# Kernel tuning notes

Hardware: AMD Instinct MI355X
Metric: run time of the kernel (lower is better)

## Reference

```python
import jax, jax.numpy as jnp
import numpy as np

NUM_HEADS = 8
CH_PER_HEAD = 40
NORM_GROUPS = 32
EPS = 1e-5


def setup_inputs() -> dict:
    key = jax.random.key(0)
    ks = jax.random.split(key, 8)
    B, C, H, W = 2, 320, 48, 48
    hid = NUM_HEADS * CH_PER_HEAD  # 320
    w_std = 0.02
    return {
        "x": jax.random.normal(ks[0], (B, C, H, W), dtype=jnp.float32),
        "gamma": jnp.ones((C,), dtype=jnp.float32),
        "beta": jnp.zeros((C,), dtype=jnp.float32),
        "Wq": jax.random.normal(ks[1], (hid, C), dtype=jnp.float32) * w_std,
        "bq": jax.random.normal(ks[2], (hid,), dtype=jnp.float32) * w_std,
        "Wk": jax.random.normal(ks[3], (hid, C), dtype=jnp.float32) * w_std,
        "bk": jax.random.normal(ks[4], (hid,), dtype=jnp.float32) * w_std,
        "Wv": jax.random.normal(ks[5], (hid, C), dtype=jnp.float32) * w_std,
        "bv": jax.random.normal(ks[6], (hid,), dtype=jnp.float32) * w_std,
        "Wo": jax.random.normal(ks[7], (C, hid), dtype=jnp.float32) * w_std,
        "bo": jnp.zeros((C,), dtype=jnp.float32),
    }


def _group_norm(x, gamma, beta):
    # x: [B, C, H, W]; GroupNorm over (C//G, H, W) per group, affine per-channel.
    B, C, H, W = x.shape
    xg = x.reshape(B, NORM_GROUPS, C // NORM_GROUPS, H, W)
    mean = xg.mean(axis=(2, 3, 4), keepdims=True)
    var = xg.var(axis=(2, 3, 4), keepdims=True)
    xn = ((xg - mean) * jax.lax.rsqrt(var + EPS)).reshape(B, C, H, W)
    return xn * gamma[None, :, None, None] + beta[None, :, None, None]


def reference(x, gamma, beta, Wq, bq, Wk, bk, Wv, bv, Wo, bo):
    B, C, H, W = x.shape
    N = H * W
    h, d = NUM_HEADS, CH_PER_HEAD
    scale = d ** (-0.25)  # applied to both q and k (net 1/sqrt(d))

    xn = _group_norm(x, gamma, beta).reshape(B, C, N)  # embedding = x_n (self-attn)

    # 1x1 Conv1d == matmul over channel dim
    q = jnp.einsum('oc,bcn->bon', Wq, xn) + bq[None, :, None]
    k = jnp.einsum('oc,bcn->bon', Wk, xn) + bk[None, :, None]
    v = jnp.einsum('oc,bcn->bon', Wv, xn) + bv[None, :, None]

    # b (h d) n -> b h d n
    q = q.reshape(B, h, d, N)
    k = k.reshape(B, h, d, N)
    v = v.reshape(B, h, d, N)

    attn = jax.nn.softmax(
        jnp.einsum('bhdi,bhdj->bhij', q * scale, k * scale), axis=-1
    )  # [B, h, N, N]
    out = jnp.einsum('bhij,bhdj->bhdi', attn, v).reshape(B, h * d, N)

    out = jnp.einsum('oc,bcn->bon', Wo, out) + bo[None, :, None]
    out = out.reshape(B, C, H, W)
    return x + out  # shapes match -> residual
```

## Files before the change

### kernel.cpp

```cpp
#include <hip/hip_runtime.h>
#include <hip/hip_bf16.h>

#define C_DIM   320
#define N_SP    2304
#define NHEADS  8
#define DHEAD   40
#define GROUPS  32
#define CPG     10
#define BATCH   2
#define DPAD    64
#define VPAD    48
#define W_ELEMS (C_DIM * C_DIM)
#define NSPLIT  3
#define TILES_PER_SPLIT 12
#define PSLOTS  41

typedef __bf16 bf16x8 __attribute__((ext_vector_type(8)));
typedef __bf16 bf16x4 __attribute__((ext_vector_type(4)));
typedef __bf16 bf16x2 __attribute__((ext_vector_type(2)));
typedef float  f32x4  __attribute__((ext_vector_type(4)));

typedef const __attribute__((address_space(1))) void* gas_ptr;
typedef __attribute__((address_space(3))) void* las_ptr;

#define MFMA16(a, b, c) __builtin_amdgcn_mfma_f32_16x16x32_bf16((a), (b), (c), 0, 0, 0)

#if __has_builtin(__builtin_amdgcn_exp2f)
#define EXP2(x) __builtin_amdgcn_exp2f(x)
#else
#define EXP2(x) __expf((x) * 0.6931471805599453f)
#endif

__device__ __forceinline__ void stage8(const char* gbase, char* lbase,
                                       int chunk, int lane)
{
    const int row = chunk * 8 + (lane >> 3);
    const int cs  = (lane & 7) * 16;
    __builtin_amdgcn_global_load_lds(
        (gas_ptr)(gbase + (size_t)row * (C_DIM * 2) + (cs ^ ((row & 7) << 4))),
        (las_ptr)(lbase + chunk * 1024 + lane * 16), 16, 0, 0);
}

__device__ __forceinline__ bf16x8 lds_frag(const char* lbase, int row, int cbyte)
{
    return *(const bf16x8*)(lbase + row * 128 + (cbyte ^ ((row & 7) << 4)));
}

__global__ __launch_bounds__(256) void prep_kernel(
    const float* __restrict__ x, float* __restrict__ partials,
    const float* __restrict__ Wq, const float* __restrict__ Wk,
    const float* __restrict__ Wv, const float* __restrict__ Wo,
    __bf16* __restrict__ Wqb, __bf16* __restrict__ Wkb,
    __bf16* __restrict__ Wvb, __bf16* __restrict__ Wob,
    __bf16* __restrict__ Qt, __bf16* __restrict__ Kt, __bf16* __restrict__ Vb)
{
    if (blockIdx.x < 512) {
        const int bid = blockIdx.x;
        const int bg = bid >> 3, p = bid & 7;
        const int b = bg >> 5, g = bg & 31;
        const float* xp = x + ((size_t)b * C_DIM + g * CPG) * N_SP + p * 288;
        const int tid = threadIdx.x;

        float sum = 0.f, sq = 0.f;
        #pragma unroll
        for (int c = 0; c < CPG; ++c) {
            for (int nl = tid; nl < 288; nl += 256) {
                const float v = xp[(size_t)c * N_SP + nl];
                sum += v; sq += v * v;
            }
        }
        #pragma unroll
        for (int off = 32; off; off >>= 1) {
            sum += __shfl_xor(sum, off);
            sq  += __shfl_xor(sq, off);
        }
        __shared__ float red[2][4];
        if ((tid & 63) == 0) { red[0][tid >> 6] = sum; red[1][tid >> 6] = sq; }
        __syncthreads();
        if (tid == 0) {
            partials[2 * bid]     = red[0][0] + red[0][1] + red[0][2] + red[0][3];
            partials[2 * bid + 1] = red[1][0] + red[1][1] + red[1][2] + red[1][3];
        }
    } else if (blockIdx.x < 612) {
        const int i = ((blockIdx.x - 512) * 256 + threadIdx.x) * 4;
        f32x4 a;
        bf16x4 o;
        a = *(const f32x4*)(Wq + i);
        #pragma unroll
        for (int e = 0; e < 4; ++e) o[e] = (__bf16)a[e];
        *(bf16x4*)(Wqb + i) = o;
        a = *(const f32x4*)(Wk + i);
        #pragma unroll
        for (int e = 0; e < 4; ++e) o[e] = (__bf16)a[e];
        *(bf16x4*)(Wkb + i) = o;
        a = *(const f32x4*)(Wv + i);
        #pragma unroll
        for (int e = 0; e < 4; ++e) o[e] = (__bf16)a[e];
        *(bf16x4*)(Wvb + i) = o;
        a = *(const f32x4*)(Wo + i);
        #pragma unroll
        for (int e = 0; e < 4; ++e) o[e] = (__bf16)a[e];
        *(bf16x4*)(Wob + i) = o;
    } else {
        const int t = (blockIdx.x - 612) * 256 + threadIdx.x;
        const bf16x8 z = {};
        __bf16* q = Qt + (size_t)t * DPAD + 40;
        __bf16* k = Kt + (size_t)t * DPAD + 40;
        *(bf16x8*)(q) = z; *(bf16x8*)(q + 8) = z; *(bf16x8*)(q + 16) = z;
        *(bf16x8*)(k) = z; *(bf16x8*)(k + 8) = z; *(bf16x8*)(k + 16) = z;
        const int bh = t / N_SP;
        const int rem = t - bh * N_SP;
        const int r = rem / 288, n8 = rem - r * 288;
        bf16x8 v = z;
        if (r == 0) {
            #pragma unroll
            for (int e = 0; e < 8; ++e) v[e] = (__bf16)1.0f;
        }
        *(bf16x8*)(Vb + ((size_t)bh * VPAD + 40 + r) * N_SP + n8 * 8) = v;
    }
}

__global__ __launch_bounds__(256) void gn_apply(
    const float* __restrict__ x,
    const float* __restrict__ gamma, const float* __restrict__ beta,
    const float* __restrict__ partials, __bf16* __restrict__ xn_t)
{
    const int bid = blockIdx.x;
    const int bg = bid >> 3, p = bid & 7;
    const int b = bg >> 5, g = bg & 31;
    const int c0 = g * CPG;

    float sum = 0.f, sq = 0.f;
    #pragma unroll
    for (int i = 0; i < 8; ++i) {
        sum += partials[(bg * 8 + i) * 2];
        sq  += partials[(bg * 8 + i) * 2 + 1];
    }
    const float inv_n = 1.0f / (float)(CPG * N_SP);
    const float mean = sum * inv_n;
    const float rstd = rsqrtf(sq * inv_n - mean * mean + 1e-5f);

    float ga[CPG], be[CPG];
    #pragma unroll
    for (int c = 0; c < CPG; ++c) {
        ga[c] = gamma[c0 + c] * rstd;
        be[c] = beta[c0 + c] - mean * ga[c];
    }

    const float* xp = x + ((size_t)b * C_DIM + c0) * N_SP + p * 288;
    for (int nl = threadIdx.x; nl < 288; nl += 256) {
        const int n = p * 288 + nl;
        __bf16* dst = xn_t + ((size_t)b * N_SP + n) * C_DIM + c0;
        #pragma unroll
        for (int j = 0; j < CPG / 2; ++j) {
            const float v0 = xp[(size_t)(2 * j) * N_SP + nl]     * ga[2 * j]     + be[2 * j];
            const float v1 = xp[(size_t)(2 * j + 1) * N_SP + nl] * ga[2 * j + 1] + be[2 * j + 1];
            bf16x2 t; t[0] = (__bf16)v0; t[1] = (__bf16)v1;
            *(bf16x2*)(dst + 2 * j) = t;
        }
    }
}

__global__ __launch_bounds__(256) void gemm_qkv(
    const __bf16* __restrict__ Wqb, const __bf16* __restrict__ Wkb, const __bf16* __restrict__ Wvb,
    const float* __restrict__ bq, const float* __restrict__ bk, const float* __restrict__ bv,
    const __bf16* __restrict__ Xt,
    __bf16* __restrict__ Qt, __bf16* __restrict__ Kt, __bf16* __restrict__ Vb)
{
    __shared__ __align__(16) char Ws[2][64 * 128];
    __shared__ __align__(16) char Xs[2][64 * 128];

    const int z = blockIdx.z;
    const int b = z / 3;
    const int which = z - 3 * b;
    const __bf16* W   = (which == 0) ? Wqb : (which == 1) ? Wkb : Wvb;
    const float* bias = (which == 0) ? bq : (which == 1) ? bk : bv;
    const float scale = (which == 0) ? 0.15811388300841897f
                      : (which == 1) ? 0.22811243f : 1.0f;

    const int n0 = blockIdx.x * 64, o0 = blockIdx.y * 64;
    const int tid = threadIdx.x, wave = tid >> 6, lane = tid & 63;
    const int lr = lane & 15, lk = lane >> 4;
    const int wm = wave >> 1, wn = wave & 1;

    const char* Wg = (const char*)(W + (size_t)o0 * C_DIM);
    const char* Xg = (const char*)(Xt + ((size_t)b * N_SP + n0) * C_DIM);

    auto stage = [&](int bufi, int s) {
        const int kb = s * 128;
        #pragma unroll
        for (int i = 0; i < 4; ++i) {
            const int c = wave * 4 + i;
            if (c < 8) stage8(Wg + kb, Ws[bufi], c, lane);
            else       stage8(Xg + kb, Xs[bufi], c - 8, lane);
        }
    };

    f32x4 acc[2][2] = {};

    stage(0, 0);
    __syncthreads();

    for (int s = 0; s < 5; ++s) {
        const int bufi = s & 1;
        if (s + 1 < 5) stage(bufi ^ 1, s + 1);

        const char* ws = Ws[bufi];
        const char* xs = Xs[bufi];
        __builtin_amdgcn_s_setprio(1);
        #pragma unroll
        for (int ksub = 0; ksub < 2; ++ksub) {
            const int cb = ksub * 64 + lk * 16;
            const bf16x8 a0 = lds_frag(ws, wm * 32 + lr,      cb);
            const bf16x8 a1 = lds_frag(ws, wm * 32 + 16 + lr, cb);
            const bf16x8 b0 = lds_frag(xs, wn * 32 + lr,      cb);
            const bf16x8 b1 = lds_frag(xs, wn * 32 + 16 + lr, cb);
            acc[0][0] = MFMA16(a0, b0, acc[0][0]);
            acc[0][1] = MFMA16(a0, b1, acc[0][1]);
            acc[1][0] = MFMA16(a1, b0, acc[1][0]);
            acc[1][1] = MFMA16(a1, b1, acc[1][1]);
        }
        __builtin_amdgcn_s_setprio(0);
        __syncthreads();
    }

    #pragma unroll
    for (int am = 0; am < 2; ++am) {
        #pragma unroll
        for (int rp = 0; rp < 2; ++rp) {
            const int o = o0 + wm * 32 + am * 16 + 4 * lk + 2 * rp;
            const int h = o / DHEAD, d = o - h * DHEAD;
            const int bh = b * NHEADS + h;
            const float b0_ = bias[o], b1_ = bias[o + 1];
            #pragma unroll
            for (int bn = 0; bn < 2; ++bn) {
                const int n = n0 + wn * 32 + bn * 16 + lr;
                const float v0 = (acc[am][bn][2 * rp]     + b0_) * scale;
                const float v1 = (acc[am][bn][2 * rp + 1] + b1_) * scale;
                if (which < 2) {
                    __bf16* dst = ((which == 0) ? Qt : Kt)
                                + ((size_t)bh * N_SP + n) * DPAD + d;
                    bf16x2 t; t[0] = (__bf16)v0; t[1] = (__bf16)v1;
                    *(bf16x2*)dst = t;
                } else {
                    Vb[((size_t)bh * VPAD + d)     * N_SP + n] = (__bf16)v0;
                    Vb[((size_t)bh * VPAD + d + 1) * N_SP + n] = (__bf16)v1;
                }
            }
        }
    }
}

__global__ __launch_bounds__(256) void gemm_out32(
    const __bf16* __restrict__ Wob, const float* __restrict__ bo,
    const __bf16* __restrict__ att_t,
    float* __restrict__ Y, const float* __restrict__ resid)
{
    __shared__ __align__(16) char Ws[2][32 * 128];
    __shared__ __align__(16) char Xs[2][64 * 128];

    const int b = blockIdx.z;
    const int n0 = blockIdx.x * 64, o0 = blockIdx.y * 32;
    const int tid = threadIdx.x, wave = tid >> 6, lane = tid & 63;
    const int lr = lane & 15, lk = lane >> 4;
    const int wn = wave;

    const char* Wg = (const char*)(Wob + (size_t)o0 * C_DIM);
    const char* Xg = (const char*)(att_t + ((size_t)b * N_SP + n0) * C_DIM);

    auto stage = [&](int bufi, int s) {
        const int kb = s * 128;
        #pragma unroll
        for (int i = 0; i < 3; ++i) {
            const int c = wave * 3 + i;
            if (c < 4) stage8(Wg + kb, Ws[bufi], c, lane);
            else       stage8(Xg + kb, Xs[bufi], c - 4, lane);
        }
    };

    f32x4 acc[2] = {};

    stage(0, 0);
    __syncthreads();

    for (int s = 0; s < 5; ++s) {
        const int bufi = s & 1;
        if (s + 1 < 5) stage(bufi ^ 1, s + 1);

        const char* ws = Ws[bufi];
        const char* xs = Xs[bufi];
        __builtin_amdgcn_s_setprio(1);
        #pragma unroll
        for (int ksub = 0; ksub < 2; ++ksub) {
            const int cb = ksub * 64 + lk * 16;
            const bf16x8 a0 = lds_frag(ws, lr,      cb);
            const bf16x8 a1 = lds_frag(ws, 16 + lr, cb);
            const bf16x8 b0 = lds_frag(xs, wn * 16 + lr, cb);
            acc[0] = MFMA16(a0, b0, acc[0]);
            acc[1] = MFMA16(a1, b0, acc[1]);
        }
        __builtin_amdgcn_s_setprio(0);
        __syncthreads();
    }

    const int n = n0 + wn * 16 + lr;
    #pragma unroll
    for (int am = 0; am < 2; ++am) {
        #pragma unroll
        for (int r = 0; r < 4; ++r) {
            const int o = o0 + am * 16 + 4 * lk + r;
            const size_t idx = ((size_t)b * C_DIM + o) * N_SP + n;
            Y[idx] = acc[am][r] + bo[o] + resid[idx];
        }
    }
}

__global__ __launch_bounds__(256, 4) void attn_mfma(
    const __bf16* __restrict__ Qt,
    const __bf16* __restrict__ Kt,
    const __bf16* __restrict__ Vb,
    __bf16* __restrict__ part)
{
    __shared__ __align__(16) __bf16 Ks[2][64 * DPAD];
    __shared__ __align__(16) __bf16 Vs[2][VPAD * 64];
    __shared__ __align__(16) __bf16 Ps[4][16 * 64];

    const int flat = blockIdx.x;
    const int bh = ((flat & 7) << 1) | ((flat >> 3) & 1);
    const int rest = flat >> 4;
    const int qx = rest / 3;
    const int s  = rest - 3 * qx;
    const int tid = threadIdx.x, wave = tid >> 6, lane = tid & 63;
    const int lr = lane & 15, lk = lane >> 4;
    const int swz = (lr & 7) << 4;
    const int i0 = (qx * 4 + wave) * 32;

    const char* Kg = (const char*)(Kt + (size_t)bh * N_SP * DPAD);
    const char* Vg = (const char*)(Vb + (size_t)bh * VPAD * N_SP);

    bf16x8 qb[2][2];
    #pragma unroll
    for (int qh = 0; qh < 2; ++qh) {
        const __bf16* Qp = Qt + ((size_t)bh * N_SP + i0 + qh * 16 + lr) * DPAD + lk * 8;
        qb[qh][0] = *(const bf16x8*)(Qp);
        qb[qh][1] = *(const bf16x8*)(Qp + 32);
    }

    f32x4 O[2][3] = {};

    auto stage = [&](char* kd, char* vd, int t) {
        const int j0 = t * 64;
        #pragma unroll
        for (int i2 = 0; i2 < 2; ++i2) {
            const int chunk = wave * 2 + i2;
            const int L = chunk * 1024 + lane * 16;
            const int src = L ^ (((L >> 7) & 7) << 4);
            __builtin_amdgcn_global_load_lds(
                (gas_ptr)(Kg + (size_t)j0 * 128 + src),
                (las_ptr)(kd + chunk * 1024), 16, 0, 0);
        }
        for (int i2 = wave; i2 < 6; i2 += 4) {
            const int row = i2 * 8 + (lane >> 3);
            const int csw = ((lane & 7) << 4) ^ ((row & 7) << 4);
            __builtin_amdgcn_global_load_lds(
                (gas_ptr)(Vg + ((size_t)row * N_SP + j0) * 2 + csw),
                (las_ptr)(vd + i2 * 1024), 16, 0, 0);
        }
    };

    auto compute = [&](const char* ks, const char* vs) {
        char* ps = (char*)Ps[wave];

        f32x4 S[2][4];
        __builtin_amdgcn_s_setprio(1);
        #pragma unroll
        for (int kt = 0; kt < 4; ++kt) {
            const int rowb = (kt * 16 + lr) * 128;
            const bf16x8 k0 = *(const bf16x8*)(ks + rowb + ((lk * 16) ^ swz));
            const bf16x8 k1 = *(const bf16x8*)(ks + rowb + ((64 + lk * 16) ^ swz));
            #pragma unroll
            for (int qh = 0; qh < 2; ++qh) {
                f32x4 zz = {};
                zz = MFMA16(k0, qb[qh][0], zz);
                S[qh][kt] = MFMA16(k1, qb[qh][1], zz);
            }
        }
        __builtin_amdgcn_s_setprio(0);

        bf16x8 va[2][3];
        #pragma unroll
        for (int hh = 0; hh < 2; ++hh)
            #pragma unroll
            for (int dt = 0; dt < 3; ++dt)
                va[hh][dt] = *(const bf16x8*)(vs + (dt * 16 + lr) * 128
                                              + ((hh * 64 + lk * 16) ^ swz));

        #pragma unroll
        for (int qh = 0; qh < 2; ++qh) {
            #pragma unroll
            for (int kt = 0; kt < 4; ++kt) {
                bf16x4 w;
                #pragma unroll
                for (int r = 0; r < 4; ++r)
                    w[r] = (__bf16)EXP2(S[qh][kt][r]);
                *(bf16x4*)(ps + lr * 128 + ((kt * 32 + lk * 8) ^ swz)) = w;
            }
            __builtin_amdgcn_s_setprio(1);
            #pragma unroll
            for (int hh = 0; hh < 2; ++hh) {
                const bf16x8 pb = *(const bf16x8*)(ps + lr * 128 + ((hh * 64 + lk * 16) ^ swz));
                #pragma unroll
                for (int dt = 0; dt < 3; ++dt)
                    O[qh][dt] = MFMA16(va[hh][dt], pb, O[qh][dt]);
            }
            __builtin_amdgcn_s_setprio(0);
        }
    };

    const int t0 = s * TILES_PER_SPLIT;

    stage((char*)Ks[0], (char*)Vs[0], t0);

    #pragma unroll 1
    for (int tt = 0; tt < TILES_PER_SPLIT; tt += 2) {
        {
            stage((char*)Ks[1], (char*)Vs[1], t0 + tt + 1);
            if (wave < 2) asm volatile("s_waitcnt vmcnt(4)" ::: "memory");
            else          asm volatile("s_waitcnt vmcnt(3)" ::: "memory");
            __builtin_amdgcn_s_barrier();
            compute((const char*)Ks[0], (const char*)Vs[0]);
            __builtin_amdgcn_s_barrier();
        }
        {
            if (tt + 2 < TILES_PER_SPLIT) {
                stage((char*)Ks[0], (char*)Vs[0], t0 + tt + 2);
                if (wave < 2) asm volatile("s_waitcnt vmcnt(4)" ::: "memory");
                else          asm volatile("s_waitcnt vmcnt(3)" ::: "memory");
            } else {
                asm volatile("s_waitcnt vmcnt(0)" ::: "memory");
            }
            __builtin_amdgcn_s_barrier();
            compute((const char*)Ks[1], (const char*)Vs[1]);
            __builtin_amdgcn_s_barrier();
        }
    }

    #pragma unroll
    for (int qh = 0; qh < 2; ++qh) {
        __bf16* pq = part + ((size_t)(s * 16 + bh) * PSLOTS) * N_SP + (i0 + qh * 16 + lr);
        #pragma unroll
        for (int dt = 0; dt < 3; ++dt) {
            #pragma unroll
            for (int r = 0; r < 4; ++r) {
                const int d = dt * 16 + 4 * lk + r;
                if (d < 40) pq[(size_t)d * N_SP] = (__bf16)O[qh][dt][r];
            }
        }
        if (lk == 2) pq[(size_t)40 * N_SP] = (__bf16)O[qh][2][0];
    }
}

__global__ __launch_bounds__(256) void attn_combine(
    const __bf16* __restrict__ part, __bf16* __restrict__ att_t)
{
    const int q  = blockIdx.x * 64 + (threadIdx.x & 63);
    const int dg = threadIdx.x >> 6;
    const int bh = blockIdx.y, b = bh >> 3, h = bh & 7;

    const __bf16* p[NSPLIT];
    float l = 0.f;
    #pragma unroll
    for (int s = 0; s < NSPLIT; ++s) {
        p[s] = part + ((size_t)(s * 16 + bh) * PSLOTS) * N_SP + q;
        l += (float)p[s][(size_t)40 * N_SP];
    }
    const float inv = 1.0f / l;

    __bf16* op = att_t + ((size_t)b * N_SP + q) * C_DIM + h * DHEAD + dg * 10;
    #pragma unroll
    for (int d = 0; d < 10; d += 2) {
        float a0 = 0.f, a1 = 0.f;
        #pragma unroll
        for (int s = 0; s < NSPLIT; ++s) {
            a0 += (float)p[s][(size_t)(dg * 10 + d)     * N_SP];
            a1 += (float)p[s][(size_t)(dg * 10 + d + 1) * N_SP];
        }
        bf16x2 t;
        t[0] = (__bf16)(a0 * inv);
        t[1] = (__bf16)(a1 * inv);
        *(bf16x2*)(op + d) = t;
    }
}

extern "C" void kernel_launch(void* const* d_in, const int* in_sizes, int n_in,
                              void* d_out, int out_size, void* d_ws, size_t ws_size,
                              hipStream_t stream) {
    const float* x     = (const float*)d_in[0];
    const float* gamma = (const float*)d_in[1];
    const float* beta  = (const float*)d_in[2];
    const float* Wq    = (const float*)d_in[3];
    const float* bq    = (const float*)d_in[4];
    const float* Wk    = (const float*)d_in[5];
    const float* bk    = (const float*)d_in[6];
    const float* Wv    = (const float*)d_in[7];
    const float* bv    = (const float*)d_in[8];
    const float* Wo    = (const float*)d_in[9];
    const float* bo    = (const float*)d_in[10];

    float* out = (float*)d_out;

    const size_t S_NC  = (size_t)BATCH * N_SP * C_DIM;
    const size_t S_QK  = (size_t)BATCH * NHEADS * N_SP * DPAD;
    const size_t S_V   = (size_t)BATCH * NHEADS * VPAD * N_SP;

    __bf16* xn_t  = (__bf16*)d_ws;
    __bf16* Qt    = xn_t + S_NC;
    __bf16* Kt    = Qt + S_QK;
    __bf16* Vb    = Kt + S_QK;
    __bf16* att_t = Vb + S_V;
    __bf16* Wqb   = att_t + S_NC;
    __bf16* Wkb   = Wqb + W_ELEMS;
    __bf16* Wvb   = Wkb + W_ELEMS;
    __bf16* Wob   = Wvb + W_ELEMS;
    float* partials = (float*)(Wob + W_ELEMS);
    __bf16* part    = (__bf16*)(partials + 1024);

    prep_kernel<<<756, 256, 0, stream>>>(
        x, partials, Wq, Wk, Wv, Wo, Wqb, Wkb, Wvb, Wob, Qt, Kt, Vb);

    gn_apply<<<512, 256, 0, stream>>>(x, gamma, beta, partials, xn_t);

    gemm_qkv<<<dim3(N_SP / 64, C_DIM / 64, 3 * BATCH), 256, 0, stream>>>(
        Wqb, Wkb, Wvb, bq, bk, bv, xn_t, Qt, Kt, Vb);

    attn_mfma<<<dim3(18 * 16 * NSPLIT), 256, 0, stream>>>(Qt, Kt, Vb, part);

    attn_combine<<<dim3(N_SP / 64, BATCH * NHEADS), 256, 0, stream>>>(part, att_t);

    gemm_out32<<<dim3(N_SP / 64, C_DIM / 32, BATCH), 256, 0, stream>>>(
        Wob, bo, att_t, out, x);
}
```

Before: 67.53 us.

## Double attention KV split count and halve KV tile to 32 keys

The attention kernel now splits the key/value sequence six ways instead of three and processes 32-key tiles instead of 64, keeping the same number of tiles per split. This doubles the number of workgroups to improve GPU occupancy and load balance, and shrinks the shared-memory footprint. The K/V staging layout, V swizzle, P scratch stride and wait counts are reworked to match the smaller tile. In exchange, there are twice as many partial results to write and combine, and less MFMA work between barriers.

```diff
diff --git a/kernel.cpp b/kernel.cpp
--- a/kernel.cpp
+++ b/kernel.cpp
@@ -11,7 +11,8 @@
 #define DPAD    64
 #define VPAD    48
 #define W_ELEMS (C_DIM * C_DIM)
-#define NSPLIT  3
+#define NSPLIT  6
+#define KVBLK   32
 #define TILES_PER_SPLIT 12
 #define PSLOTS  41
 
@@ -321,18 +322,19 @@
     const __bf16* __restrict__ Vb,
     __bf16* __restrict__ part)
 {
-    __shared__ __align__(16) __bf16 Ks[2][64 * DPAD];
-    __shared__ __align__(16) __bf16 Vs[2][VPAD * 64];
-    __shared__ __align__(16) __bf16 Ps[4][16 * 64];
+    __shared__ __align__(16) char Ks[2][KVBLK * 128];
+    __shared__ __align__(16) char Vs[2][48 * 64];
+    __shared__ __align__(16) char Ps[4][16 * 80];
 
     const int flat = blockIdx.x;
     const int bh = ((flat & 7) << 1) | ((flat >> 3) & 1);
     const int rest = flat >> 4;
-    const int qx = rest / 3;
-    const int s  = rest - 3 * qx;
+    const int qx = rest / NSPLIT;
+    const int s  = rest - NSPLIT * qx;
     const int tid = threadIdx.x, wave = tid >> 6, lane = tid & 63;
     const int lr = lane & 15, lk = lane >> 4;
     const int swz = (lr & 7) << 4;
+    const int vslot = (lk ^ ((lr >> 1) & 3)) * 16;
     const int i0 = (qx * 4 + wave) * 32;
 
     const char* Kg = (const char*)(Kt + (size_t)bh * N_SP * DPAD);
@@ -349,32 +351,30 @@
     f32x4 O[2][3] = {};
 
     auto stage = [&](char* kd, char* vd, int t) {
-        const int j0 = t * 64;
-        #pragma unroll
-        for (int i2 = 0; i2 < 2; ++i2) {
-            const int chunk = wave * 2 + i2;
-            const int L = chunk * 1024 + lane * 16;
-            const int src = L ^ (((L >> 7) & 7) << 4);
+        const int j0 = t * KVBLK;
+        {
+            const int row = wave * 8 + (lane >> 3);
+            const int cs  = (lane & 7) * 16;
             __builtin_amdgcn_global_load_lds(
-                (gas_ptr)(Kg + (size_t)j0 * 128 + src),
-                (las_ptr)(kd + chunk * 1024), 16, 0, 0);
-        }
-        for (int i2 = wave; i2 < 6; i2 += 4) {
-            const int row = i2 * 8 + (lane >> 3);
-            const int csw = ((lane & 7) << 4) ^ ((row & 7) << 4);
+                (gas_ptr)(Kg + (size_t)(j0 + row) * 128 + (cs ^ ((row & 7) << 4))),
+                (las_ptr)(kd + wave * 1024 + lane * 16), 16, 0, 0);
+        }
+        if (wave < 3) {
+            const int row = wave * 16 + (lane >> 2);
+            const int sslot = (((lane & 3) ^ ((row >> 1) & 3)) * 16);
             __builtin_amdgcn_global_load_lds(
-                (gas_ptr)(Vg + ((size_t)row * N_SP + j0) * 2 + csw),
-                (las_ptr)(vd + i2 * 1024), 16, 0, 0);
+                (gas_ptr)(Vg + (size_t)row * (N_SP * 2) + (size_t)j0 * 2 + sslot),
+                (las_ptr)(vd + wave * 1024 + lane * 16), 16, 0, 0);
         }
     };
 
     auto compute = [&](const char* ks, const char* vs) {
-        char* ps = (char*)Ps[wave];
-
-        f32x4 S[2][4];
+        char* ps = Ps[wave];
+
+        f32x4 S[2][2];
         __builtin_amdgcn_s_setprio(1);
         #pragma unroll
-        for (int kt = 0; kt < 4; ++kt) {
+        for (int kt = 0; kt < 2; ++kt) {
             const int rowb = (kt * 16 + lr) * 128;
             const bf16x8 k0 = *(const bf16x8*)(ks + rowb + ((lk * 16) ^ swz));
             const bf16x8 k1 = *(const bf16x8*)(ks + rowb + ((64 + lk * 16) ^ swz));
@@ -387,60 +387,54 @@
         }
         __builtin_amdgcn_s_setprio(0);
 
-        bf16x8 va[2][3];
-        #pragma unroll
-        for (int hh = 0; hh < 2; ++hh)
-            #pragma unroll
-            for (int dt = 0; dt < 3; ++dt)
-                va[hh][dt] = *(const bf16x8*)(vs + (dt * 16 + lr) * 128
-                                              + ((hh * 64 + lk * 16) ^ swz));
+        bf16x8 va[3];
+        #pragma unroll
+        for (int dt = 0; dt < 3; ++dt)
+            va[dt] = *(const bf16x8*)(vs + (dt * 16 + lr) * 64 + vslot);
 
         #pragma unroll
         for (int qh = 0; qh < 2; ++qh) {
             #pragma unroll
-            for (int kt = 0; kt < 4; ++kt) {
+            for (int kt = 0; kt < 2; ++kt) {
                 bf16x4 w;
                 #pragma unroll
                 for (int r = 0; r < 4; ++r)
                     w[r] = (__bf16)EXP2(S[qh][kt][r]);
-                *(bf16x4*)(ps + lr * 128 + ((kt * 32 + lk * 8) ^ swz)) = w;
+                *(bf16x4*)(ps + lr * 80 + kt * 32 + lk * 8) = w;
             }
             __builtin_amdgcn_s_setprio(1);
+            const bf16x8 pb = *(const bf16x8*)(ps + lr * 80 + lk * 16);
             #pragma unroll
-            for (int hh = 0; hh < 2; ++hh) {
-                const bf16x8 pb = *(const bf16x8*)(ps + lr * 128 + ((hh * 64 + lk * 16) ^ swz));
-                #pragma unroll
-                for (int dt = 0; dt < 3; ++dt)
-                    O[qh][dt] = MFMA16(va[hh][dt], pb, O[qh][dt]);
-            }
+            for (int dt = 0; dt < 3; ++dt)
+                O[qh][dt] = MFMA16(va[dt], pb, O[qh][dt]);
             __builtin_amdgcn_s_setprio(0);
         }
     };
 
     const int t0 = s * TILES_PER_SPLIT;
 
-    stage((char*)Ks[0], (char*)Vs[0], t0);
+    stage(Ks[0], Vs[0], t0);
 
     #pragma unroll 1
     for (int tt = 0; tt < TILES_PER_SPLIT; tt += 2) {
         {
-            stage((char*)Ks[1], (char*)Vs[1], t0 + tt + 1);
-            if (wave < 2) asm volatile("s_waitcnt vmcnt(4)" ::: "memory");
-            else          asm volatile("s_waitcnt vmcnt(3)" ::: "memory");
+            stage(Ks[1], Vs[1], t0 + tt + 1);
+            if (wave < 3) asm volatile("s_waitcnt vmcnt(2)" ::: "memory");
+            else          asm volatile("s_waitcnt vmcnt(1)" ::: "memory");
             __builtin_amdgcn_s_barrier();
-            compute((const char*)Ks[0], (const char*)Vs[0]);
+            compute(Ks[0], Vs[0]);
             __builtin_amdgcn_s_barrier();
         }
         {
             if (tt + 2 < TILES_PER_SPLIT) {
-                stage((char*)Ks[0], (char*)Vs[0], t0 + tt + 2);
-                if (wave < 2) asm volatile("s_waitcnt vmcnt(4)" ::: "memory");
-                else          asm volatile("s_waitcnt vmcnt(3)" ::: "memory");
+                stage(Ks[0], Vs[0], t0 + tt + 2);
+                if (wave < 3) asm volatile("s_waitcnt vmcnt(2)" ::: "memory");
+                else          asm volatile("s_waitcnt vmcnt(1)" ::: "memory");
             } else {
                 asm volatile("s_waitcnt vmcnt(0)" ::: "memory");
             }
             __builtin_amdgcn_s_barrier();
-            compute((const char*)Ks[1], (const char*)Vs[1]);
+            compute(Ks[1], Vs[1]);
             __builtin_amdgcn_s_barrier();
         }
     }
```

Result: no change. 68.54 us (+1.5%).
